# Performance work log

Measured on AMD Instinct MI355X. Metric: run time of the kernel, lower is better.

Reference implementation:

```python
import jax, jax.numpy as jnp
import numpy as np

B, N, DIM = 8, 4096, 512
HEADS, DIM_HEAD = 8, 64
HIDDEN = HEADS * DIM_HEAD
SCALE = DIM_HEAD ** -0.5
NEG = -1e15


def setup_inputs() -> dict:
    key = jax.random.key(0)
    k1, k2, k3, k4, k5 = jax.random.split(key, 5)
    x = jax.random.normal(k1, (B, N, DIM), dtype=jnp.float32)
    lengths = jax.random.randint(k2, (B,), 1, N + 1, dtype=jnp.int64) if jax.config.jax_enable_x64 else jax.random.randint(k2, (B,), 1, N + 1, dtype=jnp.int32)
    w_qkv = jax.random.normal(k3, (3 * HIDDEN, DIM), dtype=jnp.float32) * 0.02
    w_out = jax.random.normal(k4, (DIM, HIDDEN), dtype=jnp.float32) * 0.02
    b_out = jax.random.normal(k5, (DIM,), dtype=jnp.float32) * 0.02
    return {"x": x, "w_qkv": w_qkv, "w_out": w_out, "b_out": b_out, "lengths": lengths}


def reference(x, w_qkv, w_out, b_out, lengths):
    b, n, dim = x.shape
    # positions >= length are masked (equivalent to the cumsum trick in torch)
    pos = jnp.arange(n)
    seq_mask = pos[None, :] >= lengths[:, None]  # (b, n), True => padding

    x = jnp.where(seq_mask[:, :, None], 0.0, x)

    # pointwise Conv1d == matmul over channel dim; channels are head-major
    qkv = jnp.einsum('bnd,ed->bne', x, w_qkv)  # (b, n, 3*hidden)
    q, k, v = jnp.split(qkv, 3, axis=-1)

    def to_heads(t):  # (b, n, hidden) -> (b, heads, dim_head, n)
        return t.reshape(b, n, HEADS, DIM_HEAD).transpose(0, 2, 3, 1)

    q, k, v = to_heads(q), to_heads(k), to_heads(v)
    q = q * SCALE

    m = seq_mask[:, None, None, :]  # (b, 1, 1, n)
    q = jnp.where(m, 0.0, q)
    k = jnp.where(m, NEG, k)
    k = jax.nn.softmax(k, axis=-1)  # softmax over sequence

    context = jnp.einsum('bhdn,bhen->bhde', k, v)   # (b, h, d, d)
    out = jnp.einsum('bhde,bhdn->bhen', context, q)  # (b, h, d, n)
    out = out.transpose(0, 1, 2, 3).reshape(b, HIDDEN, n)  # (b, hidden, n), head-major
    out = jnp.einsum('bcn,dc->bdn', out, w_out) + b_out[None, :, None]
    return out.transpose(0, 2, 1)  # (b, n, dim)
```

## Files before the change

### kernel.cpp

```cpp
#include <hip/hip_runtime.h>

typedef unsigned short u16;
typedef unsigned int u32;
typedef __bf16 bf16x8 __attribute__((ext_vector_type(8)));
typedef float f32x4 __attribute__((ext_vector_type(4)));

#define L2E 1.44269504088896340736f

static __device__ __forceinline__ u16 f2bf(float f) {
  u32 u = __float_as_uint(f);
  u32 r = (u + 0x7fffu + ((u >> 16) & 1u)) >> 16;
  return (u16)r;
}
static __device__ __forceinline__ float bf2f(u32 bits) {
  return __uint_as_float(bits << 16);
}
static __device__ __forceinline__ u32 trunc_bf(float f) {
  return __float_as_uint(f) >> 16;
}

__global__ __launch_bounds__(256) void cvt_x(const float* __restrict__ src,
                                             u16* __restrict__ dst,
                                             const int* __restrict__ lengths) {
  int i = (blockIdx.x * 256 + threadIdx.x) * 8;
  int row = i >> 9;
  if ((row & 4095) >= lengths[row >> 12]) return;
  float4 a = *(const float4*)(src + i);
  float4 b = *(const float4*)(src + i + 4);
  union { u16 h[8]; uint4 v; } o;
  o.h[0] = f2bf(a.x); o.h[1] = f2bf(a.y); o.h[2] = f2bf(a.z); o.h[3] = f2bf(a.w);
  o.h[4] = f2bf(b.x); o.h[5] = f2bf(b.y); o.h[6] = f2bf(b.z); o.h[7] = f2bf(b.w);
  *(uint4*)(dst + i) = o.v;
}

__global__ __launch_bounds__(256) void prep_w(const float* __restrict__ w_qkv,
                                              u16* __restrict__ wqT,
                                              u16* __restrict__ wkvb) {
  __shared__ u16 tile[64][65];
  int bid = blockIdx.x;
  int t = threadIdx.x;
  if (bid < 64) {
    int c0 = (bid & 7) * 64, s0 = (bid >> 3) * 64;
    int r = t >> 4, cc = (t & 15) * 4;
#pragma unroll
    for (int i = 0; i < 4; ++i) {
      int row = r + i * 16;
      float4 v = *(const float4*)(w_qkv + (size_t)(c0 + row) * 512 + s0 + cc);
      tile[row][cc] = f2bf(v.x); tile[row][cc + 1] = f2bf(v.y);
      tile[row][cc + 2] = f2bf(v.z); tile[row][cc + 3] = f2bf(v.w);
    }
    __syncthreads();
#pragma unroll
    for (int i = 0; i < 4; ++i) {
      int srow = r + i * 16;
      union { u16 h[4]; uint2 u; } pk;
#pragma unroll
      for (int j = 0; j < 4; ++j) pk.h[j] = tile[cc + j][srow];
      *(uint2*)(wqT + (size_t)(s0 + srow) * 512 + c0 + cc) = pk.u;
    }
  } else {
    int i = ((bid - 64) * 256 + t) * 8;
    const float* src = w_qkv + 262144;
    float4 a = *(const float4*)(src + i);
    float4 b = *(const float4*)(src + i + 4);
    union { u16 h[8]; uint4 v; } o;
    o.h[0] = f2bf(a.x); o.h[1] = f2bf(a.y); o.h[2] = f2bf(a.z); o.h[3] = f2bf(a.w);
    o.h[4] = f2bf(b.x); o.h[5] = f2bf(b.y); o.h[6] = f2bf(b.z); o.h[7] = f2bf(b.w);
    *(uint4*)(wkvb + i) = o.v;
  }
}

template <int MODE>
__global__ __launch_bounds__(256, 4) void gemm128(const u16* __restrict__ A,
                                                  const u16* __restrict__ Bm,
                                                  u16* __restrict__ outb,
                                                  float* __restrict__ outf,
                                                  const float* __restrict__ bias,
                                                  const int* __restrict__ lengths) {
  __shared__ u16 lA[8192];
  __shared__ u16 lB[8192];

  const int t = threadIdx.x;
  const int w = t >> 6, lane = t & 63, lm = lane & 15, lg = lane >> 4;
  const int wr = w >> 1, wc = w & 1;
  const int col0 = blockIdx.y * 128;

  int row0, L = 0, myb = -1;
  if constexpr (MODE == 1) {
    row0 = blockIdx.x * 128;
  } else {
    const int pid = blockIdx.x;
    int na[8], pref = 0, panel = 0;
#pragma unroll
    for (int b = 0; b < 8; ++b) {
      int Lb = lengths[b];
      na[b] = (Lb + 127) >> 7;
      if (myb < 0 && pid < pref + na[b]) { myb = b; panel = pid - pref; L = Lb; }
      pref += na[b];
    }
    if (myb < 0) {
      if constexpr (MODE == 0) return;
      int pid2 = pid - pref, pm = 0;
#pragma unroll
      for (int b = 0; b < 8; ++b) {
        int mb = 32 - na[b];
        if (myb < 0 && pid2 < pm + mb) { myb = b; panel = na[b] + pid2 - pm; }
        pm += mb;
      }
      row0 = myb * 4096 + panel * 128;
      for (int i = t; i < 4096; i += 256) {
        int r = i >> 5, c = (i & 31) * 4;
        *(f32x4*)(outf + (size_t)(row0 + r) * 512 + col0 + c) =
            *(const f32x4*)(bias + col0 + c);
      }
      return;
    }
    row0 = myb * 4096 + panel * 128;
  }

  const u16* Abase = A + (size_t)row0 * 512;
  const u16* Bbase = Bm + (size_t)col0 * 512;
  if constexpr (MODE == 2) Bbase += (size_t)myb * 262144;

  size_t goff[4];
#pragma unroll
  for (int i = 0; i < 4; ++i) {
    int c = i * 256 + t, r = c >> 3, s = (c & 7) ^ (r & 7);
    goff[i] = (size_t)r * 512 + s * 8;
  }

  const int swz0 = (lg ^ (lm & 7)) * 8;
  const int swz1 = ((4 + lg) ^ (lm & 7)) * 8;

  f32x4 acc[4][4] = {};

  for (int kt = 0; kt < 8; ++kt) {
    const u16* sa = Abase + kt * 64;
    const u16* sb = Bbase + kt * 64;
#pragma unroll
    for (int i = 0; i < 4; ++i)
      __builtin_amdgcn_global_load_lds(
          (const __attribute__((address_space(1))) void*)(sa + goff[i]),
          (__attribute__((address_space(3))) void*)(&lA[(i * 256 + w * 64) * 8]),
          16, 0, 0);
#pragma unroll
    for (int i = 0; i < 4; ++i)
      __builtin_amdgcn_global_load_lds(
          (const __attribute__((address_space(1))) void*)(sb + goff[i]),
          (__attribute__((address_space(3))) void*)(&lB[(i * 256 + w * 64) * 8]),
          16, 0, 0);
    __syncthreads();

    const u16* la = &lA[(wr * 64 + lm) * 64];
    const u16* lb = &lB[(wc * 64 + lm) * 64];
    bf16x8 bfr[2][4];
#pragma unroll
    for (int nf = 0; nf < 4; ++nf) {
      bfr[0][nf] = *(const bf16x8*)(lb + nf * 1024 + swz0);
      bfr[1][nf] = *(const bf16x8*)(lb + nf * 1024 + swz1);
    }
#pragma unroll
    for (int mf = 0; mf < 4; ++mf) {
      bf16x8 af0 = *(const bf16x8*)(la + mf * 1024 + swz0);
      bf16x8 af1 = *(const bf16x8*)(la + mf * 1024 + swz1);
      __builtin_amdgcn_s_setprio(1);
#pragma unroll
      for (int nf = 0; nf < 4; ++nf) {
        acc[mf][nf] = __builtin_amdgcn_mfma_f32_16x16x32_bf16(
            bfr[0][nf], af0, acc[mf][nf], 0, 0, 0);
        acc[mf][nf] = __builtin_amdgcn_mfma_f32_16x16x32_bf16(
            bfr[1][nf], af1, acc[mf][nf], 0, 0, 0);
      }
      __builtin_amdgcn_s_setprio(0);
    }
    __syncthreads();
  }

  if constexpr (MODE == 0) {
    const int cls = col0 >> 9;
#pragma unroll
    for (int mf = 0; mf < 4; ++mf) {
      int grow = row0 + wr * 64 + mf * 16 + lm;
      int n = grow & 4095, bb = grow >> 12;
      bool msk = (n >= L);
#pragma unroll
      for (int nf = 0; nf < 4; ++nf) {
        int c = col0 + wc * 64 + nf * 16 + lg * 4;
        int h = (c >> 6) & 7;
        int off = (cls == 0) ? (c & 63) : (64 + (c & 63));
        f32x4 v = acc[mf][nf];
        if (msk) {
          float mv = (cls == 0) ? -1e15f : 0.f;
          v[0] = mv; v[1] = mv; v[2] = mv; v[3] = mv;
        }
        union { u16 h4[4]; uint2 u; } pk;
        pk.h4[0] = f2bf(v[0]); pk.h4[1] = f2bf(v[1]);
        pk.h4[2] = f2bf(v[2]); pk.h4[3] = f2bf(v[3]);
        *(uint2*)(outb + ((size_t)((bb * 8 + h) * 4096 + n)) * 128 + off) = pk.u;
      }
    }
  } else if constexpr (MODE == 1) {
#pragma unroll
    for (int mf = 0; mf < 4; ++mf) {
      int grow = row0 + wr * 64 + mf * 16 + lm;
      u16* rp = outb + (size_t)grow * 512 + col0 + wc * 64 + lg * 4;
#pragma unroll
      for (int nf = 0; nf < 4; ++nf) {
        f32x4 v = acc[mf][nf];
        union { u16 h4[4]; uint2 u; } pk;
        pk.h4[0] = f2bf(v[0]); pk.h4[1] = f2bf(v[1]);
        pk.h4[2] = f2bf(v[2]); pk.h4[3] = f2bf(v[3]);
        *(uint2*)(rp + nf * 16) = pk.u;
      }
    }
  } else {
    f32x4 b4[4];
#pragma unroll
    for (int nf = 0; nf < 4; ++nf)
      b4[nf] = *(const f32x4*)(bias + col0 + wc * 64 + nf * 16 + lg * 4);
#pragma unroll
    for (int mf = 0; mf < 4; ++mf) {
      int grow = row0 + wr * 64 + mf * 16 + lm;
      bool msk = ((grow & 4095) >= L);
      float* rp = outf + (size_t)grow * 512 + col0 + wc * 64 + lg * 4;
#pragma unroll
      for (int nf = 0; nf < 4; ++nf) {
        f32x4 v = msk ? b4[nf] : (acc[mf][nf] + b4[nf]);
        *(f32x4*)(rp + nf * 16) = v;
      }
    }
  }
}

struct CtxGrp {
  bf16x8 praw[2][2], vraw[2][2];
};

static __device__ __forceinline__ void ctx_load(const u16* __restrict__ base, int g,
                                                int lm, int lg, CtxGrp& X) {
  const u16* rp = base + (size_t)(g * 32 + lm) * 128 + lg * 8;
#pragma unroll
  for (int mt = 0; mt < 2; ++mt)
#pragma unroll
    for (int dh = 0; dh < 2; ++dh) {
      const u16* p = rp + mt * 2048 + dh * 32;
      X.praw[mt][dh] = *(const bf16x8*)(p);
      X.vraw[mt][dh] = *(const bf16x8*)(p + 64);
    }
}

static __device__ __forceinline__ void ctx_compute(const CtxGrp& X, bf16x8 I1, bf16x8 I2,
                                                   f32x4 acc[4][4], float sacc[4]) {
  const f32x4 zero = {0.f, 0.f, 0.f, 0.f};
  bf16x8 pf[2][2];
#pragma unroll
  for (int mt = 0; mt < 2; ++mt)
#pragma unroll
    for (int dh = 0; dh < 2; ++dh) {
      union { bf16x8 v; u32 w4[4]; } in;
      in.v = X.praw[mt][dh];
      union { u16 h[8]; bf16x8 v; } o;
#pragma unroll
      for (int i = 0; i < 4; ++i) {
        float a = bf2f(in.w4[i] & 0xffffu) * L2E;
        float bq = bf2f(in.w4[i] >> 16) * L2E;
        o.h[2 * i] = f2bf(exp2f(a));
        o.h[2 * i + 1] = f2bf(exp2f(bq));
      }
      pf[mt][dh] = o.v;
    }

  f32x4 tP[2][4], tV[2][4];
#pragma unroll
  for (int mt = 0; mt < 2; ++mt)
#pragma unroll
    for (int dh = 0; dh < 2; ++dh) {
      tP[mt][dh * 2] = __builtin_amdgcn_mfma_f32_16x16x32_bf16(pf[mt][dh], I1, zero, 0, 0, 0);
      tP[mt][dh * 2 + 1] = __builtin_amdgcn_mfma_f32_16x16x32_bf16(pf[mt][dh], I2, zero, 0, 0, 0);
      tV[mt][dh * 2] = __builtin_amdgcn_mfma_f32_16x16x32_bf16(X.vraw[mt][dh], I1, zero, 0, 0, 0);
      tV[mt][dh * 2 + 1] = __builtin_amdgcn_mfma_f32_16x16x32_bf16(X.vraw[mt][dh], I2, zero, 0, 0, 0);
    }

#pragma unroll
  for (int dt = 0; dt < 4; ++dt)
#pragma unroll
    for (int mt = 0; mt < 2; ++mt)
      sacc[dt] += tP[mt][dt][0] + tP[mt][dt][1] + tP[mt][dt][2] + tP[mt][dt][3];

  bf16x8 A2[4], B2[4];
#pragma unroll
  for (int dt = 0; dt < 4; ++dt) {
    union { u32 w4[4]; bf16x8 v; } a, bb2;
#pragma unroll
    for (int mt = 0; mt < 2; ++mt) {
      a.w4[mt * 2] = trunc_bf(tP[mt][dt][0]) | (trunc_bf(tP[mt][dt][1]) << 16);
      a.w4[mt * 2 + 1] = trunc_bf(tP[mt][dt][2]) | (trunc_bf(tP[mt][dt][3]) << 16);
      bb2.w4[mt * 2] = trunc_bf(tV[mt][dt][0]) | (trunc_bf(tV[mt][dt][1]) << 16);
      bb2.w4[mt * 2 + 1] = trunc_bf(tV[mt][dt][2]) | (trunc_bf(tV[mt][dt][3]) << 16);
    }
    A2[dt] = a.v; B2[dt] = bb2.v;
  }

#pragma unroll
  for (int dt = 0; dt < 4; ++dt)
#pragma unroll
    for (int et = 0; et < 4; ++et)
      acc[dt][et] = __builtin_amdgcn_mfma_f32_16x16x32_bf16(A2[dt], B2[et], acc[dt][et], 0, 0, 0);
}

__global__ __launch_bounds__(64, 1) void ctx_gemm(const u16* __restrict__ kvh,
                                                  float* __restrict__ ctxp,
                                                  float* __restrict__ csum,
                                                  const int* __restrict__ lengths) {
  int chunk = blockIdx.x;
  int bh = blockIdx.y;
  int b = bh >> 3;
  int L = lengths[b];
  int rows = L - chunk * 512;
  if (rows <= 0) return;
  int ng = rows >= 512 ? 16 : ((rows + 31) >> 5);

  int lane = threadIdx.x;
  int lm = lane & 15, lg = lane >> 4;

  bf16x8 I1, I2;
  {
    union { u16 h[8]; bf16x8 v; } u1, u2;
#pragma unroll
    for (int j = 0; j < 8; ++j) {
      u1.h[j] = (lg * 8 + j == lm) ? 0x3F80 : 0;
      u2.h[j] = (lg * 8 + j == lm + 16) ? 0x3F80 : 0;
    }
    I1 = u1.v; I2 = u2.v;
  }

  f32x4 acc[4][4] = {};
  float sacc[4] = {};

  const u16* base = kvh + ((size_t)bh * 4096 + (size_t)chunk * 512) * 128;

  CtxGrp A, B;
  ctx_load(base, 0, lm, lg, A);
  for (int g = 0; g < ng; g += 2) {
    if (g + 1 < ng) ctx_load(base, g + 1, lm, lg, B);
    ctx_compute(A, I1, I2, acc, sacc);
    if (g + 2 < ng) ctx_load(base, g + 2, lm, lg, A);
    if (g + 1 < ng) ctx_compute(B, I1, I2, acc, sacc);
  }

#pragma unroll
  for (int dt = 0; dt < 4; ++dt) {
    float s = sacc[dt];
    s += __shfl_xor(s, 16);
    s += __shfl_xor(s, 32);
    if (lg == 0) csum[((size_t)bh * 8 + chunk) * 64 + dt * 16 + lm] = s;
  }

  float* outp = ctxp + ((size_t)bh * 8 + chunk) * 4096;
#pragma unroll
  for (int dt = 0; dt < 4; ++dt)
#pragma unroll
    for (int et = 0; et < 4; ++et)
#pragma unroll
      for (int r = 0; r < 4; ++r)
        outp[(dt * 16 + lg * 4 + r) * 64 + et * 16 + lm] = acc[dt][et][r];
}

__global__ __launch_bounds__(256) void reduce_ctx(const float* __restrict__ ctxp,
                                                  float* __restrict__ ctxr,
                                                  const int* __restrict__ lengths) {
  int blk = blockIdx.x;
  int bh = blk >> 2, s = blk & 3;
  int nch = (lengths[bh >> 3] + 511) >> 9;
  int i = s * 1024 + threadIdx.x * 4;
  const float* p = ctxp + (size_t)bh * 8 * 4096 + i;
  f32x4 acc = {0.f, 0.f, 0.f, 0.f};
  for (int ch = 0; ch < nch; ++ch) acc += *(const f32x4*)(p + (size_t)ch * 4096);
  *(f32x4*)(ctxr + (size_t)bh * 4096 + i) = acc;
}

__global__ __launch_bounds__(256) void m_gemm(const float* __restrict__ ctxr,
                                              const float* __restrict__ csum,
                                              const float* __restrict__ w_out,
                                              u16* __restrict__ MT,
                                              const int* __restrict__ lengths) {
  int bh = blockIdx.x;
  int grp = blockIdx.y;
  int b = bh >> 3, h = bh & 7;
  int nch = (lengths[b] + 511) >> 9;
  int dd0 = grp * 128;
  int t = threadIdx.x;
  __shared__ short sctx[64 * 64];
  __shared__ short sw[128 * 64];
  {
    const float* cp = ctxr + (size_t)bh * 4096;
    int i0 = t * 16;
    int d = t >> 2;
    float den = 0.f;
    for (int ch = 0; ch < nch; ++ch) den += csum[((size_t)bh * 8 + ch) * 64 + d];
    float rin = 1.0f / den;
#pragma unroll
    for (int j = 0; j < 16; j += 4) {
      float4 v = *(const float4*)(cp + i0 + j);
      sctx[i0 + j] = (short)f2bf(v.x * rin);
      sctx[i0 + j + 1] = (short)f2bf(v.y * rin);
      sctx[i0 + j + 2] = (short)f2bf(v.z * rin);
      sctx[i0 + j + 3] = (short)f2bf(v.w * rin);
    }
  }
  {
#pragma unroll
    for (int j = 0; j < 32; j += 4) {
      int idx = t * 32 + j;
      int row = idx >> 6, col = idx & 63;
      float4 v = *(const float4*)(w_out + (size_t)(dd0 + row) * 512 + h * 64 + col);
      sw[idx] = (short)f2bf(v.x); sw[idx + 1] = (short)f2bf(v.y);
      sw[idx + 2] = (short)f2bf(v.z); sw[idx + 3] = (short)f2bf(v.w);
    }
  }
  __syncthreads();

  int lane = t & 63, w = t >> 6;
  int lm = lane & 15, lk = (lane >> 4) * 8;
  f32x4 acc[2][4] = {};
#pragma unroll
  for (int kk = 0; kk < 2; ++kk) {
    bf16x8 af[2], bfr[4];
#pragma unroll
    for (int mb = 0; mb < 2; ++mb)
      af[mb] = *(const bf16x8*)(sw + (w * 32 + mb * 16 + lm) * 64 + kk * 32 + lk);
#pragma unroll
    for (int nb = 0; nb < 4; ++nb)
      bfr[nb] = *(const bf16x8*)(sctx + (nb * 16 + lm) * 64 + kk * 32 + lk);
#pragma unroll
    for (int mb = 0; mb < 2; ++mb)
#pragma unroll
      for (int nb = 0; nb < 4; ++nb)
        acc[mb][nb] = __builtin_amdgcn_mfma_f32_16x16x32_bf16(af[mb], bfr[nb], acc[mb][nb], 0, 0, 0);
  }
  u16* outp = MT + (size_t)b * 512 * 512;
#pragma unroll
  for (int mb = 0; mb < 2; ++mb)
#pragma unroll
    for (int r = 0; r < 4; ++r) {
      int dd = dd0 + w * 32 + mb * 16 + (lane >> 4) * 4 + r;
#pragma unroll
      for (int nb = 0; nb < 4; ++nb) {
        int c = h * 64 + nb * 16 + lm;
        outp[dd * 512 + c] = f2bf(acc[mb][nb][r] * 0.125f);
      }
    }
}

extern "C" void kernel_launch(void* const* d_in, const int* in_sizes, int n_in,
                              void* d_out, int out_size, void* d_ws, size_t ws_size,
                              hipStream_t stream) {
  const float* x = (const float*)d_in[0];
  const float* w_qkv = (const float*)d_in[1];
  const float* w_out = (const float*)d_in[2];
  const float* b_out = (const float*)d_in[3];
  const int* lengths = (const int*)d_in[4];
  float* out = (float*)d_out;
  char* ws = (char*)d_ws;

  u16* kvh    = (u16*)(ws);
  u16* xb     = (u16*)(ws + 67108864);
  u16* wkvb   = (u16*)(ws + 100663296);
  u16* wqT    = (u16*)(ws + 101711872);
  float* ctxp = (float*)(ws + 102236160);
  float* csum = (float*)(ws + 110624768);
  float* ctxr = (float*)(ws + 110755840);
  u16* MT     = (u16*)(ws + 111804416);
  u16* G      = (u16*)(ws + 115998720);

  cvt_x<<<8192, 256, 0, stream>>>(x, xb, lengths);
  prep_w<<<320, 256, 0, stream>>>(w_qkv, wqT, wkvb);
  gemm128<0><<<dim3(256, 8), 256, 0, stream>>>(xb, wkvb, kvh, nullptr, nullptr, lengths);
  ctx_gemm<<<dim3(8, 64), 64, 0, stream>>>(kvh, ctxp, csum, lengths);
  reduce_ctx<<<256, 256, 0, stream>>>(ctxp, ctxr, lengths);
  m_gemm<<<dim3(64, 4), 256, 0, stream>>>(ctxr, csum, w_out, MT, lengths);
  gemm128<1><<<dim3(32, 4), 256, 0, stream>>>(MT, wqT, G, nullptr, nullptr, nullptr);
  gemm128<2><<<dim3(256, 4), 256, 0, stream>>>(xb, G, nullptr, out, b_out, lengths);
}
```

Before: 117.0 us.

## Split ctx_gemm chunk across four waves with shared-memory reduction

Each ctx_gemm block now runs four waves, and each wave handles 128 rows of the 512-row chunk instead of one wave doing all of it. Partial context and column sums are summed through shared memory before being written out. The goal is more parallelism and latency hiding on a kernel that had only 512 single-wave blocks. The cost is 64KB+ of LDS per block, a block-wide sync, and loss of the explicit double-buffered load pipeline within each wave.

```diff
diff --git a/kernel.cpp b/kernel.cpp
--- a/kernel.cpp
+++ b/kernel.cpp
@@ -308,20 +308,25 @@
       acc[dt][et] = __builtin_amdgcn_mfma_f32_16x16x32_bf16(A2[dt], B2[et], acc[dt][et], 0, 0, 0);
 }
 
-__global__ __launch_bounds__(64, 1) void ctx_gemm(const u16* __restrict__ kvh,
-                                                  float* __restrict__ ctxp,
-                                                  float* __restrict__ csum,
-                                                  const int* __restrict__ lengths) {
+__global__ __launch_bounds__(256) void ctx_gemm(const u16* __restrict__ kvh,
+                                                float* __restrict__ ctxp,
+                                                float* __restrict__ csum,
+                                                const int* __restrict__ lengths) {
   int chunk = blockIdx.x;
   int bh = blockIdx.y;
   int b = bh >> 3;
   int L = lengths[b];
   int rows = L - chunk * 512;
   if (rows <= 0) return;
-  int ng = rows >= 512 ? 16 : ((rows + 31) >> 5);
-
-  int lane = threadIdx.x;
-  int lm = lane & 15, lg = lane >> 4;
+
+  int t = threadIdx.x;
+  int w = t >> 6, lane = t & 63, lm = lane & 15, lg = lane >> 4;
+
+  int wrows = rows - w * 128;
+  int ngw = (wrows <= 0) ? 0 : (wrows >= 128 ? 4 : ((wrows + 31) >> 5));
+
+  __shared__ float red[4][4096];
+  __shared__ float redc[4][64];
 
   bf16x8 I1, I2;
   {
@@ -337,33 +342,43 @@
   f32x4 acc[4][4] = {};
   float sacc[4] = {};
 
-  const u16* base = kvh + ((size_t)bh * 4096 + (size_t)chunk * 512) * 128;
-
-  CtxGrp A, B;
-  ctx_load(base, 0, lm, lg, A);
-  for (int g = 0; g < ng; g += 2) {
-    if (g + 1 < ng) ctx_load(base, g + 1, lm, lg, B);
-    ctx_compute(A, I1, I2, acc, sacc);
-    if (g + 2 < ng) ctx_load(base, g + 2, lm, lg, A);
-    if (g + 1 < ng) ctx_compute(B, I1, I2, acc, sacc);
-  }
-
+  const u16* base = kvh + ((size_t)bh * 4096 + (size_t)chunk * 512 + (size_t)w * 128) * 128;
+
+  for (int g = 0; g < ngw; ++g) {
+    CtxGrp X;
+    ctx_load(base, g, lm, lg, X);
+    ctx_compute(X, I1, I2, acc, sacc);
+  }
+
+#pragma unroll
+  for (int dt = 0; dt < 4; ++dt)
+#pragma unroll
+    for (int et = 0; et < 4; ++et)
+#pragma unroll
+      for (int r = 0; r < 4; ++r)
+        red[w][(dt * 16 + lg * 4 + r) * 64 + et * 16 + lm] = acc[dt][et][r];
 #pragma unroll
   for (int dt = 0; dt < 4; ++dt) {
     float s = sacc[dt];
     s += __shfl_xor(s, 16);
     s += __shfl_xor(s, 32);
-    if (lg == 0) csum[((size_t)bh * 8 + chunk) * 64 + dt * 16 + lm] = s;
-  }
+    if (lg == 0) redc[w][dt * 16 + lm] = s;
+  }
+  __syncthreads();
 
   float* outp = ctxp + ((size_t)bh * 8 + chunk) * 4096;
 #pragma unroll
-  for (int dt = 0; dt < 4; ++dt)
-#pragma unroll
-    for (int et = 0; et < 4; ++et)
-#pragma unroll
-      for (int r = 0; r < 4; ++r)
-        outp[(dt * 16 + lg * 4 + r) * 64 + et * 16 + lm] = acc[dt][et][r];
+  for (int j = 0; j < 4; ++j) {
+    int i = t * 4 + j * 1024;
+    f32x4 v = *(const f32x4*)&red[0][i];
+    v += *(const f32x4*)&red[1][i];
+    v += *(const f32x4*)&red[2][i];
+    v += *(const f32x4*)&red[3][i];
+    *(f32x4*)(outp + i) = v;
+  }
+  if (t < 64)
+    csum[((size_t)bh * 8 + chunk) * 64 + t] =
+        redc[0][t] + redc[1][t] + redc[2][t] + redc[3][t];
 }
 
 __global__ __launch_bounds__(256) void reduce_ctx(const float* __restrict__ ctxp,
@@ -476,7 +491,7 @@
   cvt_x<<<8192, 256, 0, stream>>>(x, xb, lengths);
   prep_w<<<320, 256, 0, stream>>>(w_qkv, wqT, wkvb);
   gemm128<0><<<dim3(256, 8), 256, 0, stream>>>(xb, wkvb, kvh, nullptr, nullptr, lengths);
-  ctx_gemm<<<dim3(8, 64), 64, 0, stream>>>(kvh, ctxp, csum, lengths);
+  ctx_gemm<<<dim3(8, 64), 256, 0, stream>>>(kvh, ctxp, csum, lengths);
   reduce_ctx<<<256, 256, 0, stream>>>(ctxp, ctxr, lengths);
   m_gemm<<<dim3(64, 4), 256, 0, stream>>>(ctxr, csum, w_out, MT, lengths);
   gemm128<1><<<dim3(32, 4), 256, 0, stream>>>(MT, wqT, G, nullptr, nullptr, nullptr);
```

Result: faster. 107.8 us (median of 2 runs) (-7.9%).
